# Kernel optimization log

Measured on AMD Instinct MI355X. Metric: run time of the kernel, lower is better.

Reference implementation:

```python
import jax, jax.numpy as jnp
import numpy as np

B, T, C, H = 256, 256, 384, 6
HS = C // H        # 64 head size
P = int(C * 0.8)   # 307 pca_dim
EPS = 1e-6


def _rmsnorm(x, scale):
    rms = jnp.sqrt(jnp.mean(x * x, axis=-1, keepdims=True) + EPS)
    return x / rms * scale


def _orth(W):
    # torch.svd returns V (not V^T); u @ v.t() == u @ vt
    u, _, vt = jnp.linalg.svd(W, full_matrices=False)
    return u @ vt


def setup_inputs() -> dict:
    key = jax.random.key(0)
    ks = jax.random.split(key, 16)
    s = 0.02
    inp = {
        'x': jax.random.normal(ks[0], (B, T, C), jnp.float32),
        'Wq': jax.random.normal(ks[1], (H, C, HS), jnp.float32) * s,
        'Wk': jax.random.normal(ks[2], (H, C, HS), jnp.float32) * s,
        'Wv': jax.random.normal(ks[3], (H, C, HS), jnp.float32) * s,
        'Wp': jax.random.normal(ks[4], (H * HS, C), jnp.float32) * s,
        'bp': jnp.zeros((C,), jnp.float32),
        'scale1': jnp.ones((C,), jnp.float32),
        'scale2': jnp.ones((C,), jnp.float32),
        'W1': jax.random.normal(ks[5], (C, P), jnp.float32) * s,
        'b1': jnp.zeros((P,), jnp.float32),
        'W2': jax.random.normal(ks[6], (P, C), jnp.float32) * s,
        'b2': jnp.zeros((C,), jnp.float32),
        'Wo_in': jax.random.normal(ks[7], (C, C), jnp.float32),
        'Wo_out': jax.random.normal(ks[8], (C, C), jnp.float32),
    }
    return inp


def reference(x, Wq, Wk, Wv, Wp, bp, scale1, scale2, W1, b1, W2, b2, Wo_in, Wo_out):
    # ln1
    h = _rmsnorm(x, scale1)                                   # [B,T,C]
    # multi-head causal self-attention (heads batched via einsum)
    q = jnp.einsum('btc,hcd->bhtd', h, Wq)                    # [B,H,T,HS]
    k = jnp.einsum('btc,hcd->bhtd', h, Wk)
    v = jnp.einsum('btc,hcd->bhtd', h, Wv)
    wei = jnp.einsum('bhtd,bhsd->bhts', q, k) * (HS ** -0.5)  # [B,H,T,T]
    causal = jnp.tril(jnp.ones((T, T), bool))
    wei = jnp.where(causal, wei, -jnp.inf)
    wei = jax.nn.softmax(wei, axis=-1)
    attn = jnp.einsum('bhts,bhsd->bhtd', wei, v)              # [B,H,T,HS]
    attn = attn.transpose(0, 2, 1, 3).reshape(B, T, H * HS)   # concat heads
    h = attn @ Wp + bp + h                                    # residual on ln1 output
    # ln2
    h = _rmsnorm(h, scale2)
    # input orthogonal transform
    h = h @ _orth(Wo_in)
    # PCA feed-forward (dropout = identity in eval)
    h = jax.nn.relu(h @ W1 + b1)
    h = h @ W2 + b2
    # output orthogonal transform + residual on ff output
    out = h @ _orth(Wo_out) + h
    return out
```

## Files before the change

kernel.cpp:

```cpp
#include <hip/hip_runtime.h>

typedef unsigned short u16;
typedef unsigned int   u32;
typedef short s16x8 __attribute__((ext_vector_type(8)));
typedef float f32x4 __attribute__((ext_vector_type(4)));

static __device__ __forceinline__ float bf2f(u16 v){ return __uint_as_float(((u32)v)<<16); }
static __device__ __forceinline__ u16 f2bf(float f){
  u32 u = __float_as_uint(f);
  u32 r = (u + 0x7fffu + ((u>>16)&1u)) >> 16;
  return (u16)r;
}
static __device__ __forceinline__ float cvt(float v){ return v; }
static __device__ __forceinline__ float cvt(u16 v){ return bf2f(v); }
static __device__ __forceinline__ void stv(float* p, float v){ *p = v; }
static __device__ __forceinline__ void stv(u16* p, float v){ *p = f2bf(v); }

static __device__ __forceinline__ void ld2(const float* p, float& a, float& b){
  float2 t = *(const float2*)p; a=t.x; b=t.y;
}
static __device__ __forceinline__ void ld2(const u16* p, float& a, float& b){
  u32 t = *(const u32*)p; a = __uint_as_float(t<<16); b = __uint_as_float(t & 0xffff0000u);
}
static __device__ __forceinline__ void st2(float* p, float a, float b){
  float2 t; t.x=a; t.y=b; *(float2*)p = t;
}
static __device__ __forceinline__ void st2(u16* p, float a, float b){
  *(u32*)p = ((u32)f2bf(a)) | (((u32)f2bf(b))<<16);
}

static __device__ __forceinline__ void gload16(const u16* g, u16* l){
  __builtin_amdgcn_global_load_lds(
      (const __attribute__((address_space(1))) u32*)(const void*)g,
      (__attribute__((address_space(3))) u32*)(void*)l, 16, 0, 0);
}

template<typename TI, typename TO>
__global__ __launch_bounds__(256) void rms_k(const TI* __restrict__ X,
                                             const float* __restrict__ scale,
                                             TO* __restrict__ O)
{
  int row = blockIdx.x*4 + (threadIdx.x>>6);
  int lane = threadIdx.x&63;
  const TI* xr = X + (size_t)row*384;
  float v[6]; float ss = 0.f;
#pragma unroll
  for(int i=0;i<3;i++){
    ld2(xr + 2*lane + 128*i, v[2*i], v[2*i+1]);
    ss += v[2*i]*v[2*i] + v[2*i+1]*v[2*i+1];
  }
#pragma unroll
  for(int off=32; off>0; off>>=1) ss += __shfl_down(ss, off, 64);
  ss = __shfl(ss, 0, 64);
  float r = rsqrtf(ss*(1.0f/384.0f)+1e-6f);
  TO* orow = O + (size_t)row*384;
#pragma unroll
  for(int i=0;i<3;i++){
    int c = 2*lane + 128*i;
    st2(orow + c, v[2*i]*r*scale[c], v[2*i+1]*r*scale[c+1]);
  }
}

__global__ __launch_bounds__(256) void tcast_k(const float* __restrict__ In, long isz,
                                               u16* __restrict__ Out, long osz,
                                               int Rr, int Cc, int ldo)
{
  __shared__ float t[32][33];
  const int z = blockIdx.z;
  const float* I = In + (long)z*isz;
  u16* Oz = Out + (long)z*osz;
  const int r0 = blockIdx.x*32, c0 = blockIdx.y*32;
  const int tx = threadIdx.x&31, ty = threadIdx.x>>5;
#pragma unroll
  for(int rr=ty; rr<32; rr+=8){
    int r = r0+rr, c = c0+tx;
    t[rr][tx] = (r<Rr && c<Cc) ? I[(size_t)r*Cc + c] : 0.f;
  }
  __syncthreads();
#pragma unroll
  for(int cc=ty; cc<32; cc+=8){
    int c = c0+cc, r = r0+tx;
    if(c<Cc && r<ldo) Oz[(size_t)c*ldo + r] = f2bf(t[tx][cc]);
  }
}

template<int NF, typename TC, typename TR>
__global__ __launch_bounds__(256,4) void mgemm2_k(
    const u16* __restrict__ A, int lda,
    const u16* __restrict__ Bt, int ldb,
    TC* __restrict__ C, long cs_hi, int cs_lo, int csz,
    const TR* __restrict__ R,
    const float* __restrict__ bias,
    int N, int Nstore, int K, float beta, int relu, int nby)
{
  constexpr int BN = NF*32;
  __shared__ __align__(16) u16 As[128*64];
  __shared__ __align__(16) u16 Bs[BN*64];
  const int d = blockIdx.x;
  const int xcd = d&7, slot = d>>3;
  const int bm = xcd*64 + slot/nby;
  const int bn = slot - (slot/nby)*nby;
  const int m0 = bm*128, n0 = bn*BN;
  const int tid = threadIdx.x;
  const int w = tid>>6, lane = tid&63;
  const int g4 = lane>>4, l16 = lane&15;
  const int wr = w>>1, wc = w&1;
  const int srow = lane>>3;
  const int sc8  = ((lane&7) ^ srow) * 8;
  const u16* aSrc[4];
#pragma unroll
  for(int i=0;i<4;i++)
    aSrc[i] = A + (size_t)(m0 + 8*(w+4*i) + srow)*lda + sc8;
  const u16* bSrc[NF];
#pragma unroll
  for(int i=0;i<NF;i++)
    bSrc[i] = Bt + (size_t)(n0 + 8*(w+4*i) + srow)*ldb + sc8;

  f32x4 fz = {0.f,0.f,0.f,0.f};
  f32x4 acc[4][NF];
#pragma unroll
  for(int i=0;i<4;i++)
#pragma unroll
    for(int j=0;j<NF;j++) acc[i][j]=fz;

  const int sxor = l16&7;
  for(int k0=0;k0<K;k0+=64){
#pragma unroll
    for(int i=0;i<4;i++)  gload16(aSrc[i] + k0, &As[(w+4*i)*512]);
#pragma unroll
    for(int i=0;i<NF;i++) gload16(bSrc[i] + k0, &Bs[(w+4*i)*512]);
    __syncthreads();
#pragma unroll
    for(int ks=0; ks<2; ++ks){
      s16x8 av[4];
#pragma unroll
      for(int mf=0;mf<4;mf++){
        int Rr_ = wr*64 + mf*16 + l16;
        av[mf] = *(const s16x8*)&As[Rr_*64 + 8*((ks*4+g4) ^ sxor)];
      }
      s16x8 bv[NF];
#pragma unroll
      for(int nf=0;nf<NF;nf++){
        int Rn = wc*(NF*16) + nf*16 + l16;
        bv[nf] = *(const s16x8*)&Bs[Rn*64 + 8*((ks*4+g4) ^ sxor)];
      }
#pragma unroll
      for(int mf=0;mf<4;mf++)
#pragma unroll
        for(int nf=0;nf<NF;nf++)
          acc[mf][nf] = __builtin_amdgcn_mfma_f32_16x16x32_bf16(av[mf], bv[nf], acc[mf][nf], 0,0,0);
    }
    __syncthreads();
  }
#pragma unroll
  for(int mf=0;mf<4;mf++)
#pragma unroll
    for(int i=0;i<4;i++){
      int m = m0 + wr*64 + mf*16 + g4*4 + i;
      long rowoff = (long)(m>>8)*cs_hi + (long)(m&255)*cs_lo;
#pragma unroll
      for(int nf=0;nf<NF;nf++){
        int gn = n0 + wc*(NF*16) + nf*16 + l16;
        if(gn < Nstore){
          long addr = rowoff + (long)(gn>>6)*csz + (gn&63);
          float v = 0.f;
          if(gn < N){
            v = acc[mf][nf][i];
            if(R)    v += beta*cvt(R[addr]);
            if(bias) v += bias[gn];
            if(relu) v  = fmaxf(v, 0.f);
          }
          stv(C + addr, v);
        }
      }
    }
}

__global__ __launch_bounds__(256,2) void mattn_k(const u16* __restrict__ QKV,
                                                 u16* __restrict__ O)
{
  __shared__ __align__(16) u16 Ks[64*64];
  __shared__ __align__(16) u16 Vts[64*64];
  __shared__ __align__(16) u16 Ps[4*4096];
  const int bh = blockIdx.x;
  const int b = bh/6, h = bh - b*6;
  const u16* Qb = QKV + (size_t)bh*49152;
  const u16* Kb = Qb + 16384;
  const u16* Vb = Qb + 32768;
  const int tid = threadIdx.x;
  const int w = tid>>6, lane = tid&63;
  const int g4 = lane>>4, l16 = lane&15;
  char* PB = (char*)&Ps[w*4096];
  const int swz = (l16&7)<<4;

  s16x8 qf[4][2];
#pragma unroll
  for(int mi=0;mi<4;mi++)
#pragma unroll
    for(int ks=0;ks<2;ks++)
      qf[mi][ks] = *(const s16x8*)(Qb + (size_t)(w*64 + mi*16 + l16)*64 + ks*32 + g4*8);

  f32x4 fzv = {0.f,0.f,0.f,0.f};
  f32x4 o[4][4];
#pragma unroll
  for(int mf=0;mf<4;mf++)
#pragma unroll
    for(int df=0;df<4;df++) o[mf][df]=fzv;
  float mrun[4], lrun[4];
#pragma unroll
  for(int mi=0;mi<4;mi++){ mrun[mi]=-1e30f; lrun[mi]=0.f; }

  for(int st=0; st<4; ++st){
    if(st) __syncthreads();
#pragma unroll
    for(int it=0; it<2; ++it){
      int c = tid + 256*it;
      int s = c>>3, d0 = (c&7)*8;
      uint4 ld = *(const uint4*)(Kb + (size_t)(st*64+s)*64 + d0);
      int byte = s*128 + d0*2; byte ^= (s&7)<<4;
      *(uint4*)((char*)Ks + byte) = ld;
    }
#pragma unroll
    for(int it=0; it<2; ++it){
      int c = tid + 256*it;
      int s = c&63, d0 = (c>>6)*8;
      uint4 ld = *(const uint4*)(Vb + (size_t)(st*64+s)*64 + d0);
#pragma unroll
      for(int jj=0; jj<4; ++jj){
        u32 ww = (jj==0)?ld.x:(jj==1)?ld.y:(jj==2)?ld.z:ld.w;
        int d = d0 + 2*jj;
        int byte0 = d*128 + s*2;     byte0 ^= (d&7)<<4;
        int byte1 = (d+1)*128 + s*2; byte1 ^= ((d+1)&7)<<4;
        *(u16*)((char*)Vts + byte0) = (u16)(ww & 0xffffu);
        *(u16*)((char*)Vts + byte1) = (u16)(ww >> 16);
      }
    }
    __syncthreads();
    if(w < st) continue;

    f32x4 sc[4][4];
#pragma unroll
    for(int sf=0; sf<4; ++sf){
      int row = sf*16 + l16;
      s16x8 kf0 = *(const s16x8*)((char*)Ks + ((row*128 + g4*16) ^ swz));
      s16x8 kf1 = *(const s16x8*)((char*)Ks + ((row*128 + 64 + g4*16) ^ swz));
#pragma unroll
      for(int mi=0; mi<4; ++mi){
        f32x4 t = __builtin_amdgcn_mfma_f32_16x16x32_bf16(kf0, qf[mi][0], fzv, 0,0,0);
        sc[sf][mi] = __builtin_amdgcn_mfma_f32_16x16x32_bf16(kf1, qf[mi][1], t, 0,0,0);
      }
    }
    float alpha[4];
#pragma unroll
    for(int mi=0; mi<4; ++mi){
      int mloc = mi*16 + l16;
      float rmax = -3.0e38f;
#pragma unroll
      for(int sf=0; sf<4; ++sf)
#pragma unroll
        for(int i=0;i<4;i++){
          float vv = sc[sf][mi][i]*0.125f;
          if(st==w && (sf*16 + g4*4 + i) > mloc) vv = -1e30f;
          sc[sf][mi][i] = vv;
          rmax = fmaxf(rmax, vv);
        }
      rmax = fmaxf(rmax, __shfl_xor(rmax, 16, 64));
      rmax = fmaxf(rmax, __shfl_xor(rmax, 32, 64));
      float mnew = fmaxf(mrun[mi], rmax);
      float al = __expf(mrun[mi] - mnew);
      mrun[mi] = mnew;
      float ls = 0.f;
#pragma unroll
      for(int sf=0; sf<4; ++sf){
        float p0 = __expf(sc[sf][mi][0]-mnew);
        float p1 = __expf(sc[sf][mi][1]-mnew);
        float p2 = __expf(sc[sf][mi][2]-mnew);
        float p3 = __expf(sc[sf][mi][3]-mnew);
        ls += p0+p1+p2+p3;
        ushort4 pk; pk.x=f2bf(p0); pk.y=f2bf(p1); pk.z=f2bf(p2); pk.w=f2bf(p3);
        int byte = mloc*128 + sf*32 + g4*8; byte ^= (l16&7)<<4;
        *(ushort4*)(PB + byte) = pk;
      }
      ls += __shfl_xor(ls, 16, 64);
      ls += __shfl_xor(ls, 32, 64);
      lrun[mi] = lrun[mi]*al + ls;
      alpha[mi] = al;
    }
#pragma unroll
    for(int mf=0; mf<4; ++mf)
#pragma unroll
      for(int i=0;i<4;i++){
        float at = __shfl(alpha[mf], g4*4 + i, 64);
#pragma unroll
        for(int df=0; df<4; ++df) o[mf][df][i] *= at;
      }
    s16x8 vbf[4][2];
#pragma unroll
    for(int df=0; df<4; ++df){
      int row = df*16 + l16;
      vbf[df][0] = *(const s16x8*)((char*)Vts + ((row*128 + g4*16) ^ swz));
      vbf[df][1] = *(const s16x8*)((char*)Vts + ((row*128 + 64 + g4*16) ^ swz));
    }
#pragma unroll
    for(int mf=0; mf<4; ++mf){
      int row = mf*16 + l16;
      s16x8 pa0 = *(const s16x8*)(PB + ((row*128 + g4*16) ^ swz));
      s16x8 pa1 = *(const s16x8*)(PB + ((row*128 + 64 + g4*16) ^ swz));
#pragma unroll
      for(int df=0; df<4; ++df){
        f32x4 t = __builtin_amdgcn_mfma_f32_16x16x32_bf16(pa0, vbf[df][0], o[mf][df], 0,0,0);
        o[mf][df] = __builtin_amdgcn_mfma_f32_16x16x32_bf16(pa1, vbf[df][1], t, 0,0,0);
      }
    }
  }
#pragma unroll
  for(int mf=0; mf<4; ++mf)
#pragma unroll
    for(int i=0;i<4;i++){
      float lt = __shfl(lrun[mf], g4*4 + i, 64);
      float rl = 1.f/lt;
      u16* orow = O + ((size_t)(b*256 + w*64 + mf*16 + g4*4 + i))*384 + h*64;
#pragma unroll
      for(int df=0; df<4; ++df)
        orow[df*16 + l16] = f2bf(o[mf][df][i]*rl);
    }
}

__global__ __launch_bounds__(256) void fpart_k(const float* __restrict__ W0,
                                               const float* __restrict__ W1,
                                               float* __restrict__ part)
{
  int b = blockIdx.x; int z = b/24, seg = b - z*24;
  const float* W = (z ? W1 : W0) + seg*6144;
  int tid = threadIdx.x;
  float s = 0.f;
  for(int i=tid;i<6144;i+=256){ float v=W[i]; s+=v*v; }
#pragma unroll
  for(int off=32; off>0; off>>=1) s += __shfl_down(s, off, 64);
  __shared__ float red[4];
  if((tid&63)==0) red[tid>>6]=s;
  __syncthreads();
  if(tid==0) part[b] = red[0]+red[1]+red[2]+red[3];
}

__global__ __launch_bounds__(64) void fcomb_k(const float* __restrict__ part,
                                              float* __restrict__ invb)
{
  int lane = threadIdx.x;
  float v = 0.f;
  if(lane < 24) v = part[lane];
  else if(lane >= 32 && lane < 56) v = part[lane - 8];
#pragma unroll
  for(int off=1; off<32; off<<=1) v += __shfl_xor(v, off, 64);
  if(lane==0)  invb[0] = rsqrtf(v);
  if(lane==32) invb[1] = rsqrtf(v);
}

__global__ __launch_bounds__(256) void nsinit_k(const float* __restrict__ W0,
                                                const float* __restrict__ W1,
                                                const float* __restrict__ invb,
                                                u16* __restrict__ XB)
{
  int b = blockIdx.x; int z = b/24, p = b - z*24, cp0 = p*16;
  const float* W = z ? W1 : W0;
  float inv = invb[z];
  u16* base = XB + (size_t)z*589824;
  u16* xh = base;            u16* xl = base + 147456;
  u16* th = base + 294912;   u16* tl = base + 442368;
  int tid = threadIdx.x;
  for(int idx=tid; idx<6144; idx+=256){
    int r = idx>>4, j = idx&15;
    float v = W[r*384 + cp0 + j]*inv;
    u16 hh = f2bf(v);
    xh[p*6144 + idx] = hh;
    xl[p*6144 + idx] = f2bf(v - bf2f(hh));
  }
  for(int idx=tid; idx<6144; idx+=256){
    int j = idx/384, r = idx - j*384;
    float v = W[(cp0+j)*384 + r]*inv;
    u16 hh = f2bf(v);
    th[p*6144 + r*16 + j] = hh;
    tl[p*6144 + r*16 + j] = f2bf(v - bf2f(hh));
  }
}

static __device__ __forceinline__ void ns_mm2(
    const u16* __restrict__ Agh, const u16* __restrict__ Agl,
    const u16* BThL, const u16* BTlL,
    int tid, f32x4 acc[4])
{
  const int w = tid>>6, lane = tid&63, g4 = lane>>4, l16 = lane&15;
  const s16x8 z8 = {0,0,0,0,0,0,0,0};
  f32x4 fz = {0.f,0.f,0.f,0.f};
#pragma unroll
  for(int i=0;i<4;i++) acc[i]=fz;
  const bool act = (g4<2);
#pragma unroll 4
  for(int c=0;c<24;c++){
    s16x8 bh = z8, bl = z8;
    if(act){
      bh = *(const s16x8*)&BThL[l16*392 + c*16 + g4*8];
      bl = *(const s16x8*)&BTlL[l16*392 + c*16 + g4*8];
    }
#pragma unroll
    for(int tt=0;tt<4;tt++){
      const int rb = 64*w + 16*tt + l16;
      s16x8 ah = z8, al = z8;
      if(act){
        ah = *(const s16x8*)&Agh[c*6144 + rb*16 + g4*8];
        al = *(const s16x8*)&Agl[c*6144 + rb*16 + g4*8];
      }
      acc[tt] = __builtin_amdgcn_mfma_f32_16x16x32_bf16(ah, bh, acc[tt], 0,0,0);
      acc[tt] = __builtin_amdgcn_mfma_f32_16x16x32_bf16(ah, bl, acc[tt], 0,0,0);
      acc[tt] = __builtin_amdgcn_mfma_f32_16x16x32_bf16(al, bh, acc[tt], 0,0,0);
    }
  }
}

__global__ __launch_bounds__(384) void nsit_k(u16* __restrict__ XB,
                                              u16* __restrict__ QT,
                                              int it, int niter, int nq)
{
  __shared__ __align__(16) u16 BTh[16*392];
  __shared__ __align__(16) u16 BTl[16*392];
  const int blk = blockIdx.x;
  const int z = blk/24, p = blk - z*24, cp0 = p*16;
  const int tid = threadIdx.x;
  const int w = tid>>6, lane = tid&63, g4 = lane>>4, l16 = lane&15;
  const int rs = it&1;
  const u16* bin  = XB + (size_t)rs*1179648     + (size_t)z*589824;
  u16*       bout = XB + (size_t)(rs^1)*1179648 + (size_t)z*589824;
  const u16* Xh  = bin;            const u16* Xl  = bin + 147456;
  const u16* Th  = bin + 294912;   const u16* Tl  = bin + 442368;

  {
    const u16* sh = Xh + p*6144;
    const u16* sl = Xl + p*6144;
    for(int i=tid; i<768; i+=384){
      int k = i>>1, n0 = (i&1)*8;
      uint4 vh = *(const uint4*)(sh + i*8);
      uint4 vl = *(const uint4*)(sl + i*8);
#pragma unroll
      for(int j=0;j<8;j++){
        BTh[(n0+j)*392 + k] = ((u16*)&vh)[j];
        BTl[(n0+j)*392 + k] = ((u16*)&vl)[j];
      }
    }
  }
  __syncthreads();

  const bool quint = (it < nq);
  f32x4 acc[4], gsv[4];

  ns_mm2(Th, Tl, BTh, BTl, tid, acc);
  __syncthreads();
  if(quint){
#pragma unroll
    for(int tt=0;tt<4;tt++){
      gsv[tt] = acc[tt];
      int m0 = 64*w + 16*tt + g4*4;
      ushort4 h4, l4;
#pragma unroll
      for(int i=0;i<4;i++){
        float v = acc[tt][i];
        u16 hh = f2bf(v);
        ((u16*)&h4)[i]=hh; ((u16*)&l4)[i]=f2bf(v - bf2f(hh));
      }
      *(ushort4*)&BTh[l16*392 + m0] = h4;
      *(ushort4*)&BTl[l16*392 + m0] = l4;
    }
    __syncthreads();
    ns_mm2(Xh, Xl, BTh, BTl, tid, acc);
    __syncthreads();
#pragma unroll
    for(int tt=0;tt<4;tt++){
      int m0 = 64*w + 16*tt + g4*4;
      ushort4 h4, l4;
#pragma unroll
      for(int i=0;i<4;i++){
        float v = acc[tt][i];
        u16 hh = f2bf(v);
        ((u16*)&h4)[i]=hh; ((u16*)&l4)[i]=f2bf(v - bf2f(hh));
      }
      *(ushort4*)&BTh[l16*392 + m0] = h4;
      *(ushort4*)&BTl[l16*392 + m0] = l4;
    }
    __syncthreads();
    ns_mm2(Th, Tl, BTh, BTl, tid, acc);
    __syncthreads();
#pragma unroll
    for(int tt=0;tt<4;tt++){
      int m0 = 64*w + 16*tt + g4*4;
      ushort4 h4, l4;
#pragma unroll
      for(int i=0;i<4;i++){
        float v = fmaf(2.0315f, acc[tt][i], -4.7750f*(gsv[tt][i]))
                + ((m0+i)==(cp0+l16) ? 3.4445f : 0.f);
        u16 hh = f2bf(v);
        ((u16*)&h4)[i]=hh; ((u16*)&l4)[i]=f2bf(v - bf2f(hh));
      }
      *(ushort4*)&BTh[l16*392 + m0] = h4;
      *(ushort4*)&BTl[l16*392 + m0] = l4;
    }
    __syncthreads();
  } else {
#pragma unroll
    for(int tt=0;tt<4;tt++){
      int m0 = 64*w + 16*tt + g4*4;
      ushort4 h4, l4;
#pragma unroll
      for(int i=0;i<4;i++){
        float v = -0.5f*acc[tt][i] + ((m0+i)==(cp0+l16) ? 1.5f : 0.f);
        u16 hh = f2bf(v);
        ((u16*)&h4)[i]=hh; ((u16*)&l4)[i]=f2bf(v - bf2f(hh));
      }
      *(ushort4*)&BTh[l16*392 + m0] = h4;
      *(ushort4*)&BTl[l16*392 + m0] = l4;
    }
    __syncthreads();
  }
  ns_mm2(Xh, Xl, BTh, BTl, tid, acc);

  if(it == niter-1){
    u16* q = QT + (size_t)z*147456 + (size_t)(cp0+l16)*384;
#pragma unroll
    for(int tt=0;tt<4;tt++){
      int m0 = 64*w + 16*tt + g4*4;
      ushort4 h4;
#pragma unroll
      for(int i=0;i<4;i++) ((u16*)&h4)[i] = f2bf(acc[tt][i]);
      *(ushort4*)&q[m0] = h4;
    }
  } else {
    u16* oXh = bout + p*6144;            u16* oXl = bout + 147456 + p*6144;
    u16* oTh = bout + 294912;            u16* oTl = bout + 442368;
#pragma unroll
    for(int tt=0;tt<4;tt++){
      int m0 = 64*w + 16*tt + g4*4;
      ushort4 h4, l4;
#pragma unroll
      for(int i=0;i<4;i++){
        float v = acc[tt][i];
        u16 hh = f2bf(v);
        ((u16*)&h4)[i]=hh; ((u16*)&l4)[i]=f2bf(v - bf2f(hh));
        oXh[(m0+i)*16 + l16] = hh;
        oXl[(m0+i)*16 + l16] = ((u16*)&l4)[i];
      }
      size_t to = (size_t)(4*w+tt)*6144 + (size_t)(cp0+l16)*16 + g4*4;
      *(ushort4*)&oTh[to] = h4;
      *(ushort4*)&oTl[to] = l4;
    }
  }
}

extern "C" void kernel_launch(void* const* d_in, const int* in_sizes, int n_in,
                              void* d_out, int out_size, void* d_ws, size_t ws_size,
                              hipStream_t stream)
{
  const float* x      = (const float*)d_in[0];
  const float* Wq     = (const float*)d_in[1];
  const float* Wk     = (const float*)d_in[2];
  const float* Wv     = (const float*)d_in[3];
  const float* Wp     = (const float*)d_in[4];
  const float* bp     = (const float*)d_in[5];
  const float* scale1 = (const float*)d_in[6];
  const float* scale2 = (const float*)d_in[7];
  const float* W1     = (const float*)d_in[8];
  const float* b1     = (const float*)d_in[9];
  const float* W2     = (const float*)d_in[10];
  const float* b2     = (const float*)d_in[11];
  const float* Wo_in  = (const float*)d_in[12];
  const float* Wo_out = (const float*)d_in[13];

  char* ws = (char*)d_ws;
  u16* XB   = (u16*)(ws + 0);
  u16* Wqkv = (u16*)(ws + 4719104L);
  u16* WpT  = (u16*)(ws + 5603840L);
  u16* W1T  = (u16*)(ws + 5898752L);
  u16* W2T  = (u16*)(ws + 6134528L);
  u16* QT   = (u16*)(ws + 6380288L);
  float* part = (float*)(ws + 6970112L);
  float* invb = (float*)(ws + 6970496L);
  u16* h1b  = (u16*)(ws + 8388608L);
  u16* qkvb = (u16*)(ws + 58720256L);
  u16* atb  = (u16*)(ws + 209715200L);
  u16* h2b = qkvb;
  u16* h3b = qkvb + 25165824L;
  u16* h4b = qkvb + 50331648L;
  u16* h5b = atb;
  u16* h6b = h1b;

  tcast_k<<<dim3(12, 2,6),256,0,stream>>>(Wq,24576L, Wqkv,        73728L, 384, 64,384);
  tcast_k<<<dim3(12, 2,6),256,0,stream>>>(Wk,24576L, Wqkv+24576L, 73728L, 384, 64,384);
  tcast_k<<<dim3(12, 2,6),256,0,stream>>>(Wv,24576L, Wqkv+49152L, 73728L, 384, 64,384);
  tcast_k<<<dim3(12,12,1),256,0,stream>>>(Wp,0L,     WpT,0L,     384,384,384);
  tcast_k<<<dim3(12,10,1),256,0,stream>>>(W1,0L,     W1T,0L,     384,307,384);
  tcast_k<<<dim3(10,12,1),256,0,stream>>>(W2,0L,     W2T,0L,     307,384,320);

  const int NITER = 15, NQ = 10;
  fpart_k<<<48,256,0,stream>>>(Wo_in, Wo_out, part);
  fcomb_k<<<1,64,0,stream>>>(part, invb);
  nsinit_k<<<48,256,0,stream>>>(Wo_in, Wo_out, invb, XB);
  for(int it=0; it<NITER; ++it)
    nsit_k<<<48,384,0,stream>>>(XB, QT, it, NITER, NQ);

  rms_k<float,u16><<<16384,256,0,stream>>>(x, scale1, h1b);
  mgemm2_k<2,u16,float><<<9216,256,0,stream>>>(
      h1b,384,  Wqkv,384,
      qkvb, 294912L,64,16384,
      (const float*)nullptr, nullptr,
      1152,1152,384, 0.f,0, 18);
  mattn_k<<<1536,256,0,stream>>>(qkvb, atb);
  mgemm2_k<2,u16,u16><<<3072,256,0,stream>>>(
      atb,384,  WpT,384,
      h2b, 98304L,384,64,
      h1b, bp,
      384,384,384, 1.f,0, 6);
  rms_k<u16,u16><<<16384,256,0,stream>>>(h2b, scale2, h3b);
  mgemm2_k<2,u16,float><<<3072,256,0,stream>>>(
      h3b,384,  QT,384,
      h4b, 98304L,384,64,
      (const float*)nullptr, nullptr,
      384,384,384, 0.f,0, 6);
  mgemm2_k<2,u16,float><<<2560,256,0,stream>>>(
      h4b,384,  W1T,384,
      h5b, 81920L,320,64,
      (const float*)nullptr, b1,
      307,320,384, 0.f,1, 5);
  mgemm2_k<2,u16,float><<<3072,256,0,stream>>>(
      h5b,320,  W2T,320,
      h6b, 98304L,384,64,
      (const float*)nullptr, b2,
      384,384,320, 0.f,0, 6);
  mgemm2_k<2,float,u16><<<3072,256,0,stream>>>(
      h6b,384,  QT+147456,384,
      (float*)d_out, 98304L,384,64,
      h6b, nullptr,
      384,384,384, 1.f,0, 6);

  (void)in_sizes; (void)n_in; (void)ws_size; (void)out_size;
}
```

Before: 1.927 ms.

## Stage Newton-Schulz A operand through double-buffered LDS with full-K MFMA lanes

The Newton-Schulz iteration matmul used to read the A operand straight from global memory while half the lanes fed zeros, so only 16 of the 32 K elements per MFMA were real. Now each 32-wide K slab of A (hi and lo parts) is staged into a double-buffered shared-memory tile with padded rows. The next slab is prefetched into registers while MFMAs run on the current one, and all lanes supply real data, which halves the MFMA count. The cost is much more LDS per block (about 110KB), which lowers occupancy, plus an extra barrier per slab.

```diff
diff --git a/kernel.cpp b/kernel.cpp
--- a/kernel.cpp
+++ b/kernel.cpp
@@ -384,36 +384,71 @@
   }
 }
 
-static __device__ __forceinline__ void ns_mm2(
+static __device__ __forceinline__ void ns_mm4(
     const u16* __restrict__ Agh, const u16* __restrict__ Agl,
+    u16* AhL, u16* AlL,
     const u16* BThL, const u16* BTlL,
     int tid, f32x4 acc[4])
 {
   const int w = tid>>6, lane = tid&63, g4 = lane>>4, l16 = lane&15;
-  const s16x8 z8 = {0,0,0,0,0,0,0,0};
   f32x4 fz = {0.f,0.f,0.f,0.f};
 #pragma unroll
   for(int i=0;i<4;i++) acc[i]=fz;
-  const bool act = (g4<2);
-#pragma unroll 4
-  for(int c=0;c<24;c++){
-    s16x8 bh = z8, bl = z8;
-    if(act){
-      bh = *(const s16x8*)&BThL[l16*392 + c*16 + g4*8];
-      bl = *(const s16x8*)&BTlL[l16*392 + c*16 + g4*8];
-    }
+  const int r0 = tid>>1, hf = (tid&1)*8;
+  {
+#pragma unroll
+    for(int hc=0; hc<2; ++hc){
+      uint4 vh0 = *(const uint4*)(Agh + hc*6144 + tid*8);
+      uint4 vh1 = *(const uint4*)(Agh + hc*6144 + (384+tid)*8);
+      uint4 vl0 = *(const uint4*)(Agl + hc*6144 + tid*8);
+      uint4 vl1 = *(const uint4*)(Agl + hc*6144 + (384+tid)*8);
+      *(uint4*)&AhL[r0*36 + hc*16 + hf]       = vh0;
+      *(uint4*)&AhL[(r0+192)*36 + hc*16 + hf] = vh1;
+      *(uint4*)&AlL[r0*36 + hc*16 + hf]       = vl0;
+      *(uint4*)&AlL[(r0+192)*36 + hc*16 + hf] = vl1;
+    }
+  }
+  __syncthreads();
+  for(int s=0; s<12; ++s){
+    uint4 p0,p1,p2,p3,p4,p5,p6,p7;
+    if(s<11){
+      const u16* ph = Agh + (2*s+2)*6144;
+      const u16* pl = Agl + (2*s+2)*6144;
+      p0 = *(const uint4*)(ph + tid*8);
+      p1 = *(const uint4*)(ph + (384+tid)*8);
+      p2 = *(const uint4*)(ph + 6144 + tid*8);
+      p3 = *(const uint4*)(ph + 6144 + (384+tid)*8);
+      p4 = *(const uint4*)(pl + tid*8);
+      p5 = *(const uint4*)(pl + (384+tid)*8);
+      p6 = *(const uint4*)(pl + 6144 + tid*8);
+      p7 = *(const uint4*)(pl + 6144 + (384+tid)*8);
+    }
+    const u16* ah_ = AhL + (s&1)*13824;
+    const u16* al_ = AlL + (s&1)*13824;
+    s16x8 bh = *(const s16x8*)&BThL[l16*392 + s*32 + g4*8];
+    s16x8 bl = *(const s16x8*)&BTlL[l16*392 + s*32 + g4*8];
 #pragma unroll
     for(int tt=0;tt<4;tt++){
       const int rb = 64*w + 16*tt + l16;
-      s16x8 ah = z8, al = z8;
-      if(act){
-        ah = *(const s16x8*)&Agh[c*6144 + rb*16 + g4*8];
-        al = *(const s16x8*)&Agl[c*6144 + rb*16 + g4*8];
-      }
+      s16x8 ah = *(const s16x8*)&ah_[rb*36 + g4*8];
+      s16x8 al = *(const s16x8*)&al_[rb*36 + g4*8];
       acc[tt] = __builtin_amdgcn_mfma_f32_16x16x32_bf16(ah, bh, acc[tt], 0,0,0);
       acc[tt] = __builtin_amdgcn_mfma_f32_16x16x32_bf16(ah, bl, acc[tt], 0,0,0);
       acc[tt] = __builtin_amdgcn_mfma_f32_16x16x32_bf16(al, bh, acc[tt], 0,0,0);
     }
+    if(s<11){
+      u16* dh = AhL + ((s+1)&1)*13824;
+      u16* dl = AlL + ((s+1)&1)*13824;
+      *(uint4*)&dh[r0*36 + hf]            = p0;
+      *(uint4*)&dh[(r0+192)*36 + hf]      = p1;
+      *(uint4*)&dh[r0*36 + 16 + hf]       = p2;
+      *(uint4*)&dh[(r0+192)*36 + 16 + hf] = p3;
+      *(uint4*)&dl[r0*36 + hf]            = p4;
+      *(uint4*)&dl[(r0+192)*36 + hf]      = p5;
+      *(uint4*)&dl[r0*36 + 16 + hf]       = p6;
+      *(uint4*)&dl[(r0+192)*36 + 16 + hf] = p7;
+    }
+    __syncthreads();
   }
 }
 
@@ -421,6 +456,8 @@
                                               u16* __restrict__ QT,
                                               int it, int niter, int nq)
 {
+  __shared__ __align__(16) u16 AhL[2*13824];
+  __shared__ __align__(16) u16 AlL[2*13824];
   __shared__ __align__(16) u16 BTh[16*392];
   __shared__ __align__(16) u16 BTl[16*392];
   const int blk = blockIdx.x;
@@ -452,8 +489,7 @@
   const bool quint = (it < nq);
   f32x4 acc[4], gsv[4];
 
-  ns_mm2(Th, Tl, BTh, BTl, tid, acc);
-  __syncthreads();
+  ns_mm4(Th, Tl, AhL, AlL, BTh, BTl, tid, acc);
   if(quint){
 #pragma unroll
     for(int tt=0;tt<4;tt++){
@@ -470,8 +506,7 @@
       *(ushort4*)&BTl[l16*392 + m0] = l4;
     }
     __syncthreads();
-    ns_mm2(Xh, Xl, BTh, BTl, tid, acc);
-    __syncthreads();
+    ns_mm4(Xh, Xl, AhL, AlL, BTh, BTl, tid, acc);
 #pragma unroll
     for(int tt=0;tt<4;tt++){
       int m0 = 64*w + 16*tt + g4*4;
@@ -486,8 +521,7 @@
       *(ushort4*)&BTl[l16*392 + m0] = l4;
     }
     __syncthreads();
-    ns_mm2(Th, Tl, BTh, BTl, tid, acc);
-    __syncthreads();
+    ns_mm4(Th, Tl, AhL, AlL, BTh, BTl, tid, acc);
 #pragma unroll
     for(int tt=0;tt<4;tt++){
       int m0 = 64*w + 16*tt + g4*4;
@@ -519,7 +553,7 @@
     }
     __syncthreads();
   }
-  ns_mm2(Xh, Xl, BTh, BTl, tid, acc);
+  ns_mm4(Xh, Xl, AhL, AlL, BTh, BTl, tid, acc);
 
   if(it == niter-1){
     u16* q = QT + (size_t)z*147456 + (size_t)(cp0+l16)*384;
```

After: 2.315 ms. 1.2x slower.
